# Kernel tuning notes

Measured on AMD Instinct MI355X. Metric: run time of the kernel, lower is better.

## Reference

```python
import jax, jax.numpy as jnp
import numpy as np

N_NODES = 100000
N_EDGES = 1600000
IN_DIM = 128
OUT_DIM = 128


def setup_inputs() -> dict:
    key = jax.random.key(0)
    k1, k2, k3, k4, k5 = jax.random.split(key, 5)
    h = jax.random.normal(k1, (N_NODES, IN_DIM), dtype=jnp.float32)
    # nn.Linear(in_dim, out_dim): W [out, in], b [out]
    W = jax.random.normal(k2, (OUT_DIM, IN_DIM), dtype=jnp.float32) * (1.0 / np.sqrt(IN_DIM))
    b = jax.random.normal(k3, (OUT_DIM,), dtype=jnp.float32) * 0.01
    edge_src = jax.random.randint(k4, (N_EDGES,), 0, N_NODES, dtype=jnp.int32)
    edge_dst = jax.random.randint(k5, (N_EDGES,), 0, N_NODES, dtype=jnp.int32)
    return {"h": h, "W": W, "b": b, "edge_src": edge_src, "edge_dst": edge_dst}


def reference(h, W, b, edge_src, edge_dst):
    n = h.shape[0]
    # in-degree of each node (edges point src -> dst), clamped to >= 1
    deg = jax.ops.segment_sum(jnp.ones_like(edge_dst, dtype=h.dtype), edge_dst, num_segments=n)
    norm = jnp.power(jnp.clip(deg, 1.0), -0.5)[:, None]  # [N, 1]
    hn = h * norm
    # copy_u + sum: gather source features, scatter-add to destinations (SpMM)
    agg = jax.ops.segment_sum(hn[edge_src], edge_dst, num_segments=n)  # [N, in_dim]
    out = (agg * norm) @ W.T + b
    return out
```

## Files before the change

kernel.cpp:

```cpp
#include <hip/hip_runtime.h>
#include <hip/hip_fp16.h>

#define DIM 128
#define TSH 9
#define TSZ 512

typedef _Float16 half8_t __attribute__((ext_vector_type(8)));
typedef float f32x4 __attribute__((ext_vector_type(4)));


__global__ __launch_bounds__(256) void hist_a(const int* __restrict__ dst,
                                              int* __restrict__ gh,
                                              int ne, int nblk, int nt) {
    __shared__ int h[256];
    int t = threadIdx.x;
    h[t] = 0;
    __syncthreads();
    int i0 = blockIdx.x * 1024 + t;
#pragma unroll
    for (int u = 0; u < 4; ++u) {
        int i = i0 + u * 256;
        if (i < ne) atomicAdd(&h[dst[i] >> TSH], 1);
    }
    __syncthreads();
    if (t < nt) gh[t * nblk + blockIdx.x] = h[t];
}

__global__ __launch_bounds__(1024) void scan_a(int* __restrict__ g,
                                               int* __restrict__ bsum, int M) {
    __shared__ int s[1024];
    int t = threadIdx.x;
    int i = blockIdx.x * 1024 + t;
    int d = (i < M) ? g[i] : 0;
    s[t] = d;
    __syncthreads();
    for (int off = 1; off < 1024; off <<= 1) {
        int v = (t >= off) ? s[t - off] : 0;
        __syncthreads();
        s[t] += v;
        __syncthreads();
    }
    if (i < M) g[i] = s[t] - d;
    if (t == 1023) bsum[blockIdx.x] = s[1023];
}

__global__ __launch_bounds__(512) void scan_b(int* __restrict__ bsum, int nb) {
    __shared__ int s[512];
    int t = threadIdx.x;
    int d = (t < nb) ? bsum[t] : 0;
    s[t] = d;
    __syncthreads();
    for (int off = 1; off < 512; off <<= 1) {
        int v = (t >= off) ? s[t - off] : 0;
        __syncthreads();
        s[t] += v;
        __syncthreads();
    }
    if (t < nb) bsum[t] = s[t] - d;
}

__global__ __launch_bounds__(1024) void scan_c(int* __restrict__ g,
                                               const int* __restrict__ bsum, int M) {
    int i = blockIdx.x * 1024 + threadIdx.x;
    if (i < M) g[i] += bsum[blockIdx.x];
}

__global__ __launch_bounds__(256) void scatter_b(const int* __restrict__ src,
                                                 const int* __restrict__ dst,
                                                 const int* __restrict__ ghs,
                                                 unsigned* __restrict__ tbuf,
                                                 int ne, int nblk) {
    __shared__ int h[256];
    int t = threadIdx.x;
    h[t] = 0;
    __syncthreads();
    int i0 = blockIdx.x * 1024 + t;
#pragma unroll
    for (int u = 0; u < 4; ++u) {
        int i = i0 + u * 256;
        if (i < ne) {
            int d = dst[i];
            int key = d >> TSH;
            int r = atomicAdd(&h[key], 1);
            int pos = ghs[key * nblk + blockIdx.x] + r;
            tbuf[pos] = ((unsigned)src[i] << TSH) | (unsigned)(d & (TSZ - 1));
        }
    }
}

__global__ __launch_bounds__(256) void tile_sort(const unsigned* __restrict__ tbuf,
                                                 const int* __restrict__ ghs,
                                                 int* __restrict__ ebuf,
                                                 int* __restrict__ row_start,
                                                 int n, int ne, int nblk, int nt) {
    __shared__ int hist[TSZ];
    __shared__ int cur[TSZ];
    __shared__ int psum[256];
    int t = threadIdx.x;
    int tile = blockIdx.x;
    int ts = ghs[tile * nblk];
    int te = (tile + 1 < nt) ? ghs[(tile + 1) * nblk] : ne;
    hist[t] = 0;
    hist[t + 256] = 0;
    __syncthreads();
    for (int i = ts + t; i < te; i += 256)
        atomicAdd(&hist[tbuf[i] & (TSZ - 1)], 1);
    __syncthreads();
    int a = hist[2 * t], b = hist[2 * t + 1];
    psum[t] = a + b;
    __syncthreads();
    for (int off = 1; off < 256; off <<= 1) {
        int v = (t >= off) ? psum[t - off] : 0;
        __syncthreads();
        psum[t] += v;
        __syncthreads();
    }
    int e0 = psum[t] - a - b;
    cur[2 * t] = e0;
    cur[2 * t + 1] = e0 + a;
    __syncthreads();
    int node = tile * TSZ + 2 * t;
    if (node <= n) row_start[node] = ts + e0;
    if (node + 1 <= n) row_start[node + 1] = ts + e0 + a;
    for (int i = ts + t; i < te; i += 256) {
        unsigned p = tbuf[i];
        int dl = (int)(p & (TSZ - 1));
        int r = atomicAdd(&cur[dl], 1);
        ebuf[ts + r] = (int)(p >> TSH);
    }
}

__global__ __launch_bounds__(256) void hn_pack(const float* __restrict__ h,
                                               const int* __restrict__ rs,
                                               float2* __restrict__ hn, int n32) {
    int i = blockIdx.x * 256 + threadIdx.x;
    if (i >= n32) return;
    int node = i >> 5;
    int d = rs[node + 1] - rs[node];
    float sc = rsqrtf((float)(d > 1 ? d : 1));
    float4 v = ((const float4*)h)[i];
    union { __half2 h2[2]; float2 f2; } u;
    u.h2[0] = __floats2half2_rn(v.x * sc, v.y * sc);
    u.h2[1] = __floats2half2_rn(v.z * sc, v.w * sc);
    hn[i] = u.f2;
}

__global__ __launch_bounds__(256) void wprep(const float* __restrict__ W,
                                             _Float16* __restrict__ Wf) {
    int idx = blockIdx.x * 256 + threadIdx.x;
    int tile = idx >> 8;
    int kk = (idx >> 6) & 3;
    int lane = idx & 63;
    int nn = lane & 15, quad = lane >> 4;
    const float* wr = W + (tile * 16 + nn) * DIM + kk * 32 + quad * 8;
    _Float16* o = Wf + (size_t)idx * 8;
#pragma unroll
    for (int j = 0; j < 8; ++j) o[j] = (_Float16)wr[j];
}

__global__ __launch_bounds__(512) void gather_gemm(const float2* __restrict__ hn,
                                                   const int* __restrict__ ebuf,
                                                   const int* __restrict__ rs,
                                                   const _Float16* __restrict__ Wf,
                                                   const float* __restrict__ b,
                                                   float* __restrict__ out, int n) {
    __shared__ _Float16 xs[16 * 136];
    int tid = threadIdx.x;
    int g = tid >> 5, lane = tid & 31;
    int node = blockIdx.x * 16 + g;

    if (node < n) {
        int s0 = rs[node];
        int s1 = rs[node + 1];
        __half2 a0 = __floats2half2_rn(0.f, 0.f), a1 = a0;
        int i = s0;
        for (; i + 3 < s1; i += 4) {
            int e0 = ebuf[i], e1 = ebuf[i + 1], e2 = ebuf[i + 2], e3 = ebuf[i + 3];
            float2 r0 = hn[(size_t)e0 * 32 + lane];
            float2 r1 = hn[(size_t)e1 * 32 + lane];
            float2 r2 = hn[(size_t)e2 * 32 + lane];
            float2 r3 = hn[(size_t)e3 * 32 + lane];
            const __half2* q0 = (const __half2*)&r0;
            const __half2* q1 = (const __half2*)&r1;
            const __half2* q2 = (const __half2*)&r2;
            const __half2* q3 = (const __half2*)&r3;
            a0 = __hadd2(a0, q0[0]); a1 = __hadd2(a1, q0[1]);
            a0 = __hadd2(a0, q1[0]); a1 = __hadd2(a1, q1[1]);
            a0 = __hadd2(a0, q2[0]); a1 = __hadd2(a1, q2[1]);
            a0 = __hadd2(a0, q3[0]); a1 = __hadd2(a1, q3[1]);
        }
        for (; i < s1; ++i) {
            int e0 = ebuf[i];
            float2 r0 = hn[(size_t)e0 * 32 + lane];
            const __half2* q0 = (const __half2*)&r0;
            a0 = __hadd2(a0, q0[0]); a1 = __hadd2(a1, q0[1]);
        }
        int dn = s1 - s0;
        float nd = rsqrtf((float)(dn > 1 ? dn : 1));
        float2 f0 = __half22float2(a0), f1 = __half22float2(a1);
        union { __half2 h2[2]; float2 f2; } u;
        u.h2[0] = __floats2half2_rn(f0.x * nd, f0.y * nd);
        u.h2[1] = __floats2half2_rn(f1.x * nd, f1.y * nd);
        *(float2*)(xs + g * 136 + lane * 4) = u.f2;
    }
    __syncthreads();

    int w = tid >> 6;
    int wl = tid & 63;
    int cn = wl & 15;
    int quad = wl >> 4;

    f32x4 acc = {0.f, 0.f, 0.f, 0.f};
#pragma unroll
    for (int kk = 0; kk < 4; ++kk) {
        half8_t af = *(const half8_t*)(xs + cn * 136 + kk * 32 + quad * 8);
        half8_t bf = ((const half8_t*)Wf)[(w * 4 + kk) * 64 + wl];
        acc = __builtin_amdgcn_mfma_f32_16x16x32_f16(af, bf, acc, 0, 0, 0);
    }
    float bj = b[w * 16 + cn];
    int node0 = blockIdx.x * 16;
#pragma unroll
    for (int r = 0; r < 4; ++r) {
        int row = quad * 4 + r;
        if (node0 + row < n)
            out[(size_t)(node0 + row) * DIM + w * 16 + cn] = acc[r] + bj;
    }
}

extern "C" void kernel_launch(void* const* d_in, const int* in_sizes, int n_in,
                              void* d_out, int out_size, void* d_ws, size_t ws_size,
                              hipStream_t stream) {
    const float* h = (const float*)d_in[0];
    const float* W = (const float*)d_in[1];
    const float* b = (const float*)d_in[2];
    const int* esrc = (const int*)d_in[3];
    const int* edst = (const int*)d_in[4];
    float* out = (float*)d_out;

    int n = in_sizes[0] / DIM;
    int ne = in_sizes[3];

    int nblk = (ne + 1023) / 1024;
    int nt = (n + TSZ - 1) >> TSH;
    int M = nt * nblk;
    int nsc = (M + 1023) / 1024;

    float2* hn = (float2*)d_ws;
    _Float16* Wf = (_Float16*)(hn + (size_t)n * 32);
    int* row_start = (int*)(Wf + 16384);
    int* gh = row_start + (n + 1);
    int* gbsum = gh + M;
    unsigned* tbuf = (unsigned*)(gbsum + 512);
    int* ebuf = (int*)(tbuf + ne);

    hist_a<<<nblk, 256, 0, stream>>>(edst, gh, ne, nblk, nt);
    scan_a<<<nsc, 1024, 0, stream>>>(gh, gbsum, M);
    scan_b<<<1, 512, 0, stream>>>(gbsum, nsc);
    scan_c<<<nsc, 1024, 0, stream>>>(gh, gbsum, M);
    scatter_b<<<nblk, 256, 0, stream>>>(esrc, edst, gh, tbuf, ne, nblk);
    tile_sort<<<nt, 256, 0, stream>>>(tbuf, gh, ebuf, row_start, n, ne, nblk, nt);
    wprep<<<8, 256, 0, stream>>>(W, Wf);
    hn_pack<<<(n * 32 + 255) / 256, 256, 0, stream>>>(h, row_start, hn, n * 32);
    gather_gemm<<<(n + 15) / 16, 512, 0, stream>>>(hn, ebuf, row_start, Wf, b, out, n);
}
```

Before: 251.9 us.

## Shrink sort tiles, merge scan kernels, and process 64 nodes per gather block

Halves the destination tile size to 256 nodes and raises edges per histogram block to 4096, cutting the number of histogram entries. The three-pass scan becomes a wave-shuffle scan plus a combined block-sum scan and weight-prep kernel, and the scan_c pass is dropped by adding block sums at use sites. The gather-GEMM kernel now handles 64 nodes per block, with a deeper 8-way gather unroll and reuse of each W fragment across four MFMA row tiles. This trades fewer launches and better W reuse for larger shared memory per block and longer serial gathers per warp.

```diff
diff --git a/kernel.cpp b/kernel.cpp
--- a/kernel.cpp
+++ b/kernel.cpp
@@ -2,8 +2,9 @@
 #include <hip/hip_fp16.h>
 
 #define DIM 128
-#define TSH 9
-#define TSZ 512
+#define TSH 8
+#define TSZ 256
+#define EBLK 4096
 
 typedef _Float16 half8_t __attribute__((ext_vector_type(8)));
 typedef float f32x4 __attribute__((ext_vector_type(4)));
@@ -12,116 +13,146 @@
 __global__ __launch_bounds__(256) void hist_a(const int* __restrict__ dst,
                                               int* __restrict__ gh,
                                               int ne, int nblk, int nt) {
-    __shared__ int h[256];
+    __shared__ int h[512];
     int t = threadIdx.x;
-    h[t] = 0;
-    __syncthreads();
-    int i0 = blockIdx.x * 1024 + t;
-#pragma unroll
-    for (int u = 0; u < 4; ++u) {
+    h[t] = 0; h[t + 256] = 0;
+    __syncthreads();
+    int i0 = blockIdx.x * EBLK + t;
+#pragma unroll
+    for (int u = 0; u < 16; ++u) {
         int i = i0 + u * 256;
         if (i < ne) atomicAdd(&h[dst[i] >> TSH], 1);
     }
     __syncthreads();
-    if (t < nt) gh[t * nblk + blockIdx.x] = h[t];
-}
-
-__global__ __launch_bounds__(1024) void scan_a(int* __restrict__ g,
-                                               int* __restrict__ bsum, int M) {
-    __shared__ int s[1024];
+    for (int k = t; k < nt; k += 256) gh[k * nblk + blockIdx.x] = h[k];
+}
+
+__global__ __launch_bounds__(256) void scan_a(int* __restrict__ g,
+                                              int* __restrict__ bsum, int M) {
+    __shared__ int wsum[4];
     int t = threadIdx.x;
-    int i = blockIdx.x * 1024 + t;
-    int d = (i < M) ? g[i] : 0;
-    s[t] = d;
-    __syncthreads();
-    for (int off = 1; off < 1024; off <<= 1) {
-        int v = (t >= off) ? s[t - off] : 0;
+    int base = blockIdx.x * 1024 + t * 4;
+    int4 v;
+    if (base + 3 < M) v = *(const int4*)(g + base);
+    else {
+        v.x = (base + 0 < M) ? g[base + 0] : 0;
+        v.y = (base + 1 < M) ? g[base + 1] : 0;
+        v.z = (base + 2 < M) ? g[base + 2] : 0;
+        v.w = (base + 3 < M) ? g[base + 3] : 0;
+    }
+    int s3 = v.x + v.y + v.z + v.w;
+    int lane = t & 63, wv = t >> 6;
+    int x = s3;
+#pragma unroll
+    for (int off = 1; off < 64; off <<= 1) {
+        int y = __shfl_up(x, off, 64);
+        if (lane >= off) x += y;
+    }
+    if (lane == 63) wsum[wv] = x;
+    __syncthreads();
+    int woff = 0;
+    for (int i = 0; i < wv; ++i) woff += wsum[i];
+    int ex = woff + x - s3;
+    int4 o;
+    o.x = ex; o.y = ex + v.x; o.z = o.y + v.y; o.w = o.z + v.z;
+    if (base + 3 < M) *(int4*)(g + base) = o;
+    else {
+        if (base + 0 < M) g[base + 0] = o.x;
+        if (base + 1 < M) g[base + 1] = o.y;
+        if (base + 2 < M) g[base + 2] = o.z;
+        if (base + 3 < M) g[base + 3] = o.w;
+    }
+    if (t == 0) bsum[blockIdx.x] = wsum[0] + wsum[1] + wsum[2] + wsum[3];
+}
+
+__global__ __launch_bounds__(256) void scanb_wprep(int* __restrict__ bsum, int nb,
+                                                   const float* __restrict__ W,
+                                                   _Float16* __restrict__ Wf) {
+    if (blockIdx.x == 0) {
+        __shared__ int s[256];
+        int t = threadIdx.x;
+        int d = (t < nb) ? bsum[t] : 0;
+        s[t] = d;
         __syncthreads();
-        s[t] += v;
-        __syncthreads();
-    }
-    if (i < M) g[i] = s[t] - d;
-    if (t == 1023) bsum[blockIdx.x] = s[1023];
-}
-
-__global__ __launch_bounds__(512) void scan_b(int* __restrict__ bsum, int nb) {
-    __shared__ int s[512];
-    int t = threadIdx.x;
-    int d = (t < nb) ? bsum[t] : 0;
-    s[t] = d;
-    __syncthreads();
-    for (int off = 1; off < 512; off <<= 1) {
-        int v = (t >= off) ? s[t - off] : 0;
-        __syncthreads();
-        s[t] += v;
-        __syncthreads();
-    }
-    if (t < nb) bsum[t] = s[t] - d;
-}
-
-__global__ __launch_bounds__(1024) void scan_c(int* __restrict__ g,
-                                               const int* __restrict__ bsum, int M) {
-    int i = blockIdx.x * 1024 + threadIdx.x;
-    if (i < M) g[i] += bsum[blockIdx.x];
+        for (int off = 1; off < 256; off <<= 1) {
+            int v = (t >= off) ? s[t - off] : 0;
+            __syncthreads();
+            s[t] += v;
+            __syncthreads();
+        }
+        if (t < nb) bsum[t] = s[t] - d;
+    } else {
+        int idx = (blockIdx.x - 1) * 256 + threadIdx.x;
+        int tile = idx >> 8;
+        int kk = (idx >> 6) & 3;
+        int lane = idx & 63;
+        int nn = lane & 15, quad = lane >> 4;
+        const float* wr = W + (tile * 16 + nn) * DIM + kk * 32 + quad * 8;
+        _Float16* o = Wf + (size_t)idx * 8;
+#pragma unroll
+        for (int j = 0; j < 8; ++j) o[j] = (_Float16)wr[j];
+    }
 }
 
 __global__ __launch_bounds__(256) void scatter_b(const int* __restrict__ src,
                                                  const int* __restrict__ dst,
-                                                 const int* __restrict__ ghs,
+                                                 const int* __restrict__ gh,
+                                                 const int* __restrict__ gb,
                                                  unsigned* __restrict__ tbuf,
                                                  int ne, int nblk) {
-    __shared__ int h[256];
+    __shared__ int h[512];
     int t = threadIdx.x;
-    h[t] = 0;
-    __syncthreads();
-    int i0 = blockIdx.x * 1024 + t;
-#pragma unroll
-    for (int u = 0; u < 4; ++u) {
+    h[t] = 0; h[t + 256] = 0;
+    __syncthreads();
+    int i0 = blockIdx.x * EBLK + t;
+#pragma unroll
+    for (int u = 0; u < 16; ++u) {
         int i = i0 + u * 256;
         if (i < ne) {
             int d = dst[i];
             int key = d >> TSH;
             int r = atomicAdd(&h[key], 1);
-            int pos = ghs[key * nblk + blockIdx.x] + r;
+            int idx = key * nblk + blockIdx.x;
+            int pos = gh[idx] + gb[idx >> 10] + r;
             tbuf[pos] = ((unsigned)src[i] << TSH) | (unsigned)(d & (TSZ - 1));
         }
     }
 }
 
 __global__ __launch_bounds__(256) void tile_sort(const unsigned* __restrict__ tbuf,
-                                                 const int* __restrict__ ghs,
+                                                 const int* __restrict__ gh,
+                                                 const int* __restrict__ gb,
                                                  int* __restrict__ ebuf,
                                                  int* __restrict__ row_start,
                                                  int n, int ne, int nblk, int nt) {
     __shared__ int hist[TSZ];
     __shared__ int cur[TSZ];
-    __shared__ int psum[256];
+    __shared__ int ps[TSZ];
     int t = threadIdx.x;
     int tile = blockIdx.x;
-    int ts = ghs[tile * nblk];
-    int te = (tile + 1 < nt) ? ghs[(tile + 1) * nblk] : ne;
+    int i0 = tile * nblk;
+    int ts = gh[i0] + gb[i0 >> 10];
+    int i1 = (tile + 1) * nblk;
+    int te = (tile + 1 < nt) ? gh[i1] + gb[i1 >> 10] : ne;
     hist[t] = 0;
-    hist[t + 256] = 0;
     __syncthreads();
     for (int i = ts + t; i < te; i += 256)
         atomicAdd(&hist[tbuf[i] & (TSZ - 1)], 1);
     __syncthreads();
-    int a = hist[2 * t], b = hist[2 * t + 1];
-    psum[t] = a + b;
+    int d = hist[t];
+    ps[t] = d;
     __syncthreads();
     for (int off = 1; off < 256; off <<= 1) {
-        int v = (t >= off) ? psum[t - off] : 0;
+        int v = (t >= off) ? ps[t - off] : 0;
         __syncthreads();
-        psum[t] += v;
+        ps[t] += v;
         __syncthreads();
     }
-    int e0 = psum[t] - a - b;
-    cur[2 * t] = e0;
-    cur[2 * t + 1] = e0 + a;
-    __syncthreads();
-    int node = tile * TSZ + 2 * t;
-    if (node <= n) row_start[node] = ts + e0;
-    if (node + 1 <= n) row_start[node + 1] = ts + e0 + a;
+    int ex = ps[t] - d;
+    cur[t] = ex;
+    int node = tile * TSZ + t;
+    if (node <= n) row_start[node] = ts + ex;
+    __syncthreads();
     for (int i = ts + t; i < te; i += 256) {
         unsigned p = tbuf[i];
         int dl = (int)(p & (TSZ - 1));
@@ -145,63 +176,85 @@
     hn[i] = u.f2;
 }
 
-__global__ __launch_bounds__(256) void wprep(const float* __restrict__ W,
-                                             _Float16* __restrict__ Wf) {
-    int idx = blockIdx.x * 256 + threadIdx.x;
-    int tile = idx >> 8;
-    int kk = (idx >> 6) & 3;
-    int lane = idx & 63;
-    int nn = lane & 15, quad = lane >> 4;
-    const float* wr = W + (tile * 16 + nn) * DIM + kk * 32 + quad * 8;
-    _Float16* o = Wf + (size_t)idx * 8;
-#pragma unroll
-    for (int j = 0; j < 8; ++j) o[j] = (_Float16)wr[j];
-}
-
 __global__ __launch_bounds__(512) void gather_gemm(const float2* __restrict__ hn,
                                                    const int* __restrict__ ebuf,
                                                    const int* __restrict__ rs,
                                                    const _Float16* __restrict__ Wf,
                                                    const float* __restrict__ b,
                                                    float* __restrict__ out, int n) {
-    __shared__ _Float16 xs[16 * 136];
+    __shared__ _Float16 xs[64 * 136];
     int tid = threadIdx.x;
     int g = tid >> 5, lane = tid & 31;
-    int node = blockIdx.x * 16 + g;
-
-    if (node < n) {
-        int s0 = rs[node];
-        int s1 = rs[node + 1];
-        __half2 a0 = __floats2half2_rn(0.f, 0.f), a1 = a0;
-        int i = s0;
-        for (; i + 3 < s1; i += 4) {
-            int e0 = ebuf[i], e1 = ebuf[i + 1], e2 = ebuf[i + 2], e3 = ebuf[i + 3];
-            float2 r0 = hn[(size_t)e0 * 32 + lane];
-            float2 r1 = hn[(size_t)e1 * 32 + lane];
-            float2 r2 = hn[(size_t)e2 * 32 + lane];
-            float2 r3 = hn[(size_t)e3 * 32 + lane];
-            const __half2* q0 = (const __half2*)&r0;
-            const __half2* q1 = (const __half2*)&r1;
-            const __half2* q2 = (const __half2*)&r2;
-            const __half2* q3 = (const __half2*)&r3;
-            a0 = __hadd2(a0, q0[0]); a1 = __hadd2(a1, q0[1]);
-            a0 = __hadd2(a0, q1[0]); a1 = __hadd2(a1, q1[1]);
-            a0 = __hadd2(a0, q2[0]); a1 = __hadd2(a1, q2[1]);
-            a0 = __hadd2(a0, q3[0]); a1 = __hadd2(a1, q3[1]);
-        }
-        for (; i < s1; ++i) {
-            int e0 = ebuf[i];
-            float2 r0 = hn[(size_t)e0 * 32 + lane];
-            const __half2* q0 = (const __half2*)&r0;
-            a0 = __hadd2(a0, q0[0]); a1 = __hadd2(a1, q0[1]);
-        }
-        int dn = s1 - s0;
-        float nd = rsqrtf((float)(dn > 1 ? dn : 1));
-        float2 f0 = __half22float2(a0), f1 = __half22float2(a1);
+
+#pragma unroll
+    for (int it = 0; it < 4; ++it) {
+        int row = it * 16 + g;
+        int node = blockIdx.x * 64 + row;
         union { __half2 h2[2]; float2 f2; } u;
-        u.h2[0] = __floats2half2_rn(f0.x * nd, f0.y * nd);
-        u.h2[1] = __floats2half2_rn(f1.x * nd, f1.y * nd);
-        *(float2*)(xs + g * 136 + lane * 4) = u.f2;
+        if (node < n) {
+            int s0 = rs[node];
+            int s1 = rs[node + 1];
+            __half2 a0 = __floats2half2_rn(0.f, 0.f), a1 = a0;
+            int i = s0;
+            for (; i + 7 < s1; i += 8) {
+                int e0 = ebuf[i], e1 = ebuf[i + 1], e2 = ebuf[i + 2], e3 = ebuf[i + 3];
+                int e4 = ebuf[i + 4], e5 = ebuf[i + 5], e6 = ebuf[i + 6], e7 = ebuf[i + 7];
+                float2 r0 = hn[(size_t)e0 * 32 + lane];
+                float2 r1 = hn[(size_t)e1 * 32 + lane];
+                float2 r2 = hn[(size_t)e2 * 32 + lane];
+                float2 r3 = hn[(size_t)e3 * 32 + lane];
+                float2 r4 = hn[(size_t)e4 * 32 + lane];
+                float2 r5 = hn[(size_t)e5 * 32 + lane];
+                float2 r6 = hn[(size_t)e6 * 32 + lane];
+                float2 r7 = hn[(size_t)e7 * 32 + lane];
+                const __half2* q0 = (const __half2*)&r0;
+                const __half2* q1 = (const __half2*)&r1;
+                const __half2* q2 = (const __half2*)&r2;
+                const __half2* q3 = (const __half2*)&r3;
+                const __half2* q4 = (const __half2*)&r4;
+                const __half2* q5 = (const __half2*)&r5;
+                const __half2* q6 = (const __half2*)&r6;
+                const __half2* q7 = (const __half2*)&r7;
+                a0 = __hadd2(a0, q0[0]); a1 = __hadd2(a1, q0[1]);
+                a0 = __hadd2(a0, q1[0]); a1 = __hadd2(a1, q1[1]);
+                a0 = __hadd2(a0, q2[0]); a1 = __hadd2(a1, q2[1]);
+                a0 = __hadd2(a0, q3[0]); a1 = __hadd2(a1, q3[1]);
+                a0 = __hadd2(a0, q4[0]); a1 = __hadd2(a1, q4[1]);
+                a0 = __hadd2(a0, q5[0]); a1 = __hadd2(a1, q5[1]);
+                a0 = __hadd2(a0, q6[0]); a1 = __hadd2(a1, q6[1]);
+                a0 = __hadd2(a0, q7[0]); a1 = __hadd2(a1, q7[1]);
+            }
+            for (; i + 3 < s1; i += 4) {
+                int e0 = ebuf[i], e1 = ebuf[i + 1], e2 = ebuf[i + 2], e3 = ebuf[i + 3];
+                float2 r0 = hn[(size_t)e0 * 32 + lane];
+                float2 r1 = hn[(size_t)e1 * 32 + lane];
+                float2 r2 = hn[(size_t)e2 * 32 + lane];
+                float2 r3 = hn[(size_t)e3 * 32 + lane];
+                const __half2* q0 = (const __half2*)&r0;
+                const __half2* q1 = (const __half2*)&r1;
+                const __half2* q2 = (const __half2*)&r2;
+                const __half2* q3 = (const __half2*)&r3;
+                a0 = __hadd2(a0, q0[0]); a1 = __hadd2(a1, q0[1]);
+                a0 = __hadd2(a0, q1[0]); a1 = __hadd2(a1, q1[1]);
+                a0 = __hadd2(a0, q2[0]); a1 = __hadd2(a1, q2[1]);
+                a0 = __hadd2(a0, q3[0]); a1 = __hadd2(a1, q3[1]);
+            }
+            for (; i < s1; ++i) {
+                int e0 = ebuf[i];
+                float2 r0 = hn[(size_t)e0 * 32 + lane];
+                const __half2* q0 = (const __half2*)&r0;
+                a0 = __hadd2(a0, q0[0]); a1 = __hadd2(a1, q0[1]);
+            }
+            int dn = s1 - s0;
+            float nd = rsqrtf((float)(dn > 1 ? dn : 1));
+            float2 f0 = __half22float2(a0), f1 = __half22float2(a1);
+            u.h2[0] = __floats2half2_rn(f0.x * nd, f0.y * nd);
+            u.h2[1] = __floats2half2_rn(f1.x * nd, f1.y * nd);
+        } else {
+            u.h2[0] = __floats2half2_rn(0.f, 0.f);
+            u.h2[1] = u.h2[0];
+        }
+        *(float2*)(xs + row * 136 + lane * 4) = u.f2;
     }
     __syncthreads();
 
@@ -210,20 +263,27 @@
     int cn = wl & 15;
     int quad = wl >> 4;
 
-    f32x4 acc = {0.f, 0.f, 0.f, 0.f};
+    f32x4 acc[4] = {{0.f, 0.f, 0.f, 0.f}, {0.f, 0.f, 0.f, 0.f},
+                    {0.f, 0.f, 0.f, 0.f}, {0.f, 0.f, 0.f, 0.f}};
 #pragma unroll
     for (int kk = 0; kk < 4; ++kk) {
-        half8_t af = *(const half8_t*)(xs + cn * 136 + kk * 32 + quad * 8);
         half8_t bf = ((const half8_t*)Wf)[(w * 4 + kk) * 64 + wl];
-        acc = __builtin_amdgcn_mfma_f32_16x16x32_f16(af, bf, acc, 0, 0, 0);
+#pragma unroll
+        for (int rt = 0; rt < 4; ++rt) {
+            half8_t af = *(const half8_t*)(xs + (rt * 16 + cn) * 136 + kk * 32 + quad * 8);
+            acc[rt] = __builtin_amdgcn_mfma_f32_16x16x32_f16(af, bf, acc[rt], 0, 0, 0);
+        }
     }
     float bj = b[w * 16 + cn];
-    int node0 = blockIdx.x * 16;
-#pragma unroll
-    for (int r = 0; r < 4; ++r) {
-        int row = quad * 4 + r;
-        if (node0 + row < n)
-            out[(size_t)(node0 + row) * DIM + w * 16 + cn] = acc[r] + bj;
+    int node0 = blockIdx.x * 64;
+#pragma unroll
+    for (int rt = 0; rt < 4; ++rt) {
+#pragma unroll
+        for (int r = 0; r < 4; ++r) {
+            int node = node0 + rt * 16 + quad * 4 + r;
+            if (node < n)
+                out[(size_t)node * DIM + w * 16 + cn] = acc[rt][r] + bj;
+        }
     }
 }
 
@@ -240,7 +300,7 @@
     int n = in_sizes[0] / DIM;
     int ne = in_sizes[3];
 
-    int nblk = (ne + 1023) / 1024;
+    int nblk = (ne + EBLK - 1) / EBLK;
     int nt = (n + TSZ - 1) >> TSH;
     int M = nt * nblk;
     int nsc = (M + 1023) / 1024;
@@ -250,16 +310,14 @@
     int* row_start = (int*)(Wf + 16384);
     int* gh = row_start + (n + 1);
     int* gbsum = gh + M;
-    unsigned* tbuf = (unsigned*)(gbsum + 512);
+    unsigned* tbuf = (unsigned*)(gbsum + 256);
     int* ebuf = (int*)(tbuf + ne);
 
     hist_a<<<nblk, 256, 0, stream>>>(edst, gh, ne, nblk, nt);
-    scan_a<<<nsc, 1024, 0, stream>>>(gh, gbsum, M);
-    scan_b<<<1, 512, 0, stream>>>(gbsum, nsc);
-    scan_c<<<nsc, 1024, 0, stream>>>(gh, gbsum, M);
-    scatter_b<<<nblk, 256, 0, stream>>>(esrc, edst, gh, tbuf, ne, nblk);
-    tile_sort<<<nt, 256, 0, stream>>>(tbuf, gh, ebuf, row_start, n, ne, nblk, nt);
-    wprep<<<8, 256, 0, stream>>>(W, Wf);
+    scan_a<<<nsc, 256, 0, stream>>>(gh, gbsum, M);
+    scanb_wprep<<<9, 256, 0, stream>>>(gbsum, nsc, W, Wf);
+    scatter_b<<<nblk, 256, 0, stream>>>(esrc, edst, gh, gbsum, tbuf, ne, nblk);
+    tile_sort<<<nt, 256, 0, stream>>>(tbuf, gh, gbsum, ebuf, row_start, n, ne, nblk, nt);
     hn_pack<<<(n * 32 + 255) / 256, 256, 0, stream>>>(h, row_start, hn, n * 32);
-    gather_gemm<<<(n + 15) / 16, 512, 0, stream>>>(hn, ebuf, row_start, Wf, b, out, n);
-}
+    gather_gemm<<<(n + 63) / 64, 512, 0, stream>>>(hn, ebuf, row_start, Wf, b, out, n);
+}
```

Result: faster. 233.5 us (-7.3%).
